# Optimization experiments

Measured on AMD Instinct MI355X. Metric: run time of the kernel, lower is better.

Reference implementation:

```python
import jax, jax.numpy as jnp
import numpy as np

N, E, D, H, DH, M = 100000, 1600000, 128, 8, 16, 3  # nodes, edges, model_dim, heads, head_dim, views
NEG = -1e9


def setup_inputs() -> dict:
    key = jax.random.key(0)
    ks = jax.random.split(key, 12)
    x = jax.random.normal(ks[0], (N, D), jnp.float32)
    src = jax.random.randint(ks[1], (E,), 0, N)
    dst = jax.random.randint(ks[2], (E,), 0, N)
    pi = jax.random.uniform(ks[3], (N, H, M), jnp.float32)
    pi = pi / pi.sum(-1, keepdims=True)  # router mixture over views
    view_w = jax.random.uniform(ks[4], (E, M), jnp.float32)
    s = 1.0 / np.sqrt(D)
    Wq = jax.random.normal(ks[5], (D, D), jnp.float32) * s
    Wk = jax.random.normal(ks[6], (D, D), jnp.float32) * s
    Wv = jax.random.normal(ks[7], (D, D), jnp.float32) * s
    bq = jax.random.normal(ks[8], (D,), jnp.float32) * 0.02
    bk = jax.random.normal(ks[9], (D,), jnp.float32) * 0.02
    bv = jax.random.normal(ks[10], (D,), jnp.float32) * 0.02
    return {"x": x, "pi": pi, "view_w": view_w, "Wq": Wq, "bq": bq,
            "Wk": Wk, "bk": bk, "Wv": Wv, "bv": bv, "src": src, "dst": dst}


def reference(x, pi, view_w, Wq, bq, Wk, bk, Wv, bv, src, dst):
    n = x.shape[0]
    q = (x @ Wq + bq).reshape(n, H, DH)
    k = (x @ Wk + bk).reshape(n, H, DH)
    v = (x @ Wv + bv).reshape(n, H, DH)
    # per-edge mixture weight: sum over views of pi[dst] * view_w  -> [E, H]
    mix = jnp.einsum('ehm,em->eh', pi[dst], view_w)
    raw = jnp.einsum('ehd,ehd->eh', q[dst], k[src]) / jnp.sqrt(jnp.float32(DH))
    scores = raw + jnp.log(jnp.clip(mix, 1e-8))  # adjacency_mode == 'bias'
    valid = mix > 0
    masked = jnp.where(valid, scores, NEG)
    # scatter-softmax over incoming edges per (node, head)
    smax = jax.ops.segment_max(masked, dst, num_segments=n)
    expv = jnp.where(valid, jnp.exp(masked - smax[dst]), 0.0)
    ssum = jax.ops.segment_sum(expv, dst, num_segments=n)
    attn = expv / jnp.maximum(ssum[dst], 1e-8)  # [E, H]
    # weighted scatter-sum aggregation -> [N, H, DH]
    node_states = jax.ops.segment_sum(v[src] * attn[:, :, None], dst, num_segments=n)
    return node_states, attn
```

## Files before the change

### kernel.cpp

```cpp
#include <hip/hip_runtime.h>
#include <hip/hip_bf16.h>
#include <math.h>

#define NEG -1e9f
#define SCAN_CHUNK 2048

typedef _Float16 half8 __attribute__((ext_vector_type(8)));
typedef _Float16 half16v __attribute__((ext_vector_type(16)));
typedef float floatx4 __attribute__((ext_vector_type(4)));


__global__ void hist_kernel(const int* __restrict__ dst, int* __restrict__ counts, int e) {
    int i = blockIdx.x * blockDim.x + threadIdx.x;
    if (i < e) atomicAdd(&counts[dst[i]], 1);
}

__global__ __launch_bounds__(256) void scan_block_sums(const int* __restrict__ counts,
                                                       int* __restrict__ bsum, int n) {
    __shared__ int sd[256];
    int t = threadIdx.x;
    int base = blockIdx.x * SCAN_CHUNK + t * 8;
    int s = 0;
#pragma unroll
    for (int j = 0; j < 8; ++j) {
        int idx = base + j;
        if (idx < n) s += counts[idx];
    }
    sd[t] = s;
    __syncthreads();
    for (int off = 128; off > 0; off >>= 1) {
        if (t < off) sd[t] += sd[t + off];
        __syncthreads();
    }
    if (t == 0) bsum[blockIdx.x] = sd[0];
}

__global__ void scan_wave(int* bsum, int nb) {
    int lane = threadIdx.x;
    int orig = (lane < nb) ? bsum[lane] : 0;
    int v = orig;
    for (int off = 1; off < 64; off <<= 1) {
        int t = __shfl_up(v, off, 64);
        if (lane >= off) v += t;
    }
    if (lane < nb) bsum[lane] = v - orig;
}

__global__ __launch_bounds__(256) void scan_write(const int* __restrict__ counts,
                                                  const int* __restrict__ bsum,
                                                  int* __restrict__ row_ptr,
                                                  int* __restrict__ cursor,
                                                  int n, int total) {
    __shared__ int sd[256];
    int t = threadIdx.x;
    int base = blockIdx.x * SCAN_CHUNK + t * 8;
    int v[8];
    int s = 0;
#pragma unroll
    for (int j = 0; j < 8; ++j) {
        int idx = base + j;
        v[j] = (idx < n) ? counts[idx] : 0;
        s += v[j];
    }
    sd[t] = s;
    __syncthreads();
    for (int off = 1; off < 256; off <<= 1) {
        int tmp = 0;
        if (t >= off) tmp = sd[t - off];
        __syncthreads();
        if (t >= off) sd[t] += tmp;
        __syncthreads();
    }
    int run = bsum[blockIdx.x] + sd[t] - s;
#pragma unroll
    for (int j = 0; j < 8; ++j) {
        int idx = base + j;
        if (idx < n) {
            row_ptr[idx] = run;
            cursor[idx] = run;
            run += v[j];
        }
    }
    if (blockIdx.x == 0 && t == 0) row_ptr[n] = total;
}

__global__ void fill_csr(const int* __restrict__ dst, int* cursor,
                         int* __restrict__ csr, int e) {
    int i = blockIdx.x * blockDim.x + threadIdx.x;
    if (i < e) {
        int p = atomicAdd(&cursor[dst[i]], 1);
        csr[p] = i;
    }
}


__global__ __launch_bounds__(256) void convert_x(const float* __restrict__ x,
                                                 _Float16* __restrict__ xh, int total8) {
    int i = blockIdx.x * blockDim.x + threadIdx.x;
    if (i < total8) {
        const float4* s = (const float4*)x + i * 2;
        float4 a = s[0], b = s[1];
        half8 h;
        h[0] = (_Float16)a.x; h[1] = (_Float16)a.y; h[2] = (_Float16)a.z; h[3] = (_Float16)a.w;
        h[4] = (_Float16)b.x; h[5] = (_Float16)b.y; h[6] = (_Float16)b.z; h[7] = (_Float16)b.w;
        *((half8*)xh + i) = h;
    }
}

__global__ __launch_bounds__(256) void prep_w(const float* __restrict__ Wq,
                                              const float* __restrict__ Wk,
                                              const float* __restrict__ Wv,
                                              _Float16* __restrict__ wt) {
    const float* W = (blockIdx.x == 0) ? Wq : (blockIdx.x == 1) ? Wk : Wv;
    _Float16* out = wt + (size_t)blockIdx.x * 16384;
    int t = threadIdx.x;
    for (int r = 0; r < 64; ++r) {
        int idx = r * 256 + t;
        int k = idx >> 7, nn = idx & 127;
        out[nn * 128 + k] = (_Float16)W[idx];
    }
}


#define LDP 136

__global__ __launch_bounds__(256) void qkv_mfma(
    const _Float16* __restrict__ xh, const _Float16* __restrict__ wt,
    const float* __restrict__ bq, const float* __restrict__ bk,
    const float* __restrict__ bv,
    _Float16* __restrict__ qh, _Float16* __restrict__ kh, _Float16* __restrict__ vh,
    int n) {
    __shared__ __align__(16) _Float16 xs[128 * LDP];
    __shared__ __align__(16) _Float16 ws[128 * LDP];

    int t = threadIdx.x;
    int tile0 = blockIdx.x * 128;
    int sel = blockIdx.y;
    const _Float16* wsel = wt + (size_t)sel * 16384;
    const float* bias = (sel == 0) ? bq : (sel == 1) ? bk : bv;
    _Float16* out = (sel == 0) ? qh : (sel == 1) ? kh : vh;

#pragma unroll
    for (int r = 0; r < 8; ++r) {
        int id = r * 256 + t;
        int row = id >> 4, c8 = id & 15;
        int grow = tile0 + row;
        half8 val = (half8)(_Float16)0;
        if (grow < n) val = *((const half8*)(xh + (size_t)grow * 128) + c8);
        *((half8*)(xs + row * LDP) + c8) = val;
        half8 wv = *((const half8*)(wsel + row * 128) + c8);
        *((half8*)(ws + row * LDP) + c8) = wv;
    }
    __syncthreads();

    int wave = t >> 6, lane = t & 63;
    int wm = (wave & 1) * 64, wn = (wave >> 1) * 64;
    int lrow = lane & 15, quad = lane >> 4;

    floatx4 acc[4][4];
#pragma unroll
    for (int i = 0; i < 4; ++i)
#pragma unroll
        for (int j = 0; j < 4; ++j) acc[i][j] = (floatx4)0.f;

#pragma unroll
    for (int kk = 0; kk < 4; ++kk) {
        int kbase = kk * 32 + quad * 8;
        half8 a[4], b[4];
#pragma unroll
        for (int i = 0; i < 4; ++i)
            a[i] = *(const half8*)(xs + (wm + i * 16 + lrow) * LDP + kbase);
#pragma unroll
        for (int j = 0; j < 4; ++j)
            b[j] = *(const half8*)(ws + (wn + j * 16 + lrow) * LDP + kbase);
#pragma unroll
        for (int i = 0; i < 4; ++i)
#pragma unroll
            for (int j = 0; j < 4; ++j)
                acc[i][j] = __builtin_amdgcn_mfma_f32_16x16x32_f16(a[i], b[j], acc[i][j], 0, 0, 0);
    }

#pragma unroll
    for (int i = 0; i < 4; ++i) {
#pragma unroll
        for (int j = 0; j < 4; ++j) {
            int col = wn + j * 16 + lrow;
            float bv_ = bias[col];
#pragma unroll
            for (int r = 0; r < 4; ++r) {
                int row = wm + i * 16 + quad * 4 + r;
                int grow = tile0 + row;
                if (grow < n) out[(size_t)grow * 128 + col] = (_Float16)(acc[i][j][r] + bv_);
            }
        }
    }
}


__global__ __launch_bounds__(256) void edge_attn(
    const _Float16* __restrict__ qh, const _Float16* __restrict__ kh,
    const _Float16* __restrict__ vh, const float* __restrict__ pi,
    const float* __restrict__ view_w, const int* __restrict__ src,
    const int* __restrict__ row_ptr, const int* __restrict__ csr,
    float* __restrict__ node_out, float* attn_out, int n) {
    int t = threadIdx.x;
    int node = blockIdx.x * 32 + (t >> 3);
    int h = t & 7;
    if (node >= n) return;

    half16v qv = *(const half16v*)(qh + (size_t)node * 128 + h * 16);
    float qf[16];
#pragma unroll
    for (int j = 0; j < 16; ++j) qf[j] = (float)qv[j];

    float p0 = pi[node * 24 + h * 3 + 0];
    float p1 = pi[node * 24 + h * 3 + 1];
    float p2 = pi[node * 24 + h * 3 + 2];
    int beg = row_ptr[node], end = row_ptr[node + 1];

    float m = -INFINITY, l = 0.f;
    float acc[16];
#pragma unroll
    for (int j = 0; j < 16; ++j) acc[j] = 0.f;

    for (int i = beg; i < end; ++i) {
        int e = csr[i];
        int s0 = src[e];
        float w0 = view_w[e * 3 + 0], w1 = view_w[e * 3 + 1], w2 = view_w[e * 3 + 2];
        float mix = fmaf(p0, w0, fmaf(p1, w1, p2 * w2));
        half16v kv = *(const half16v*)(kh + (size_t)s0 * 128 + h * 16);
        float dot = 0.f;
#pragma unroll
        for (int j = 0; j < 16; ++j) dot = fmaf(qf[j], (float)kv[j], dot);
        float s = (mix > 0.f) ? (dot * 0.25f + __logf(fmaxf(mix, 1e-8f))) : NEG;
        attn_out[(size_t)e * 8 + h] = s;
        if (s > 0.5f * NEG) {
            if (s > m) {
                float sc = __expf(m - s);
                l *= sc;
#pragma unroll
                for (int j = 0; j < 16; ++j) acc[j] *= sc;
                m = s;
            }
            float w = __expf(s - m);
            l += w;
            half16v vv = *(const half16v*)(vh + (size_t)s0 * 128 + h * 16);
#pragma unroll
            for (int j = 0; j < 16; ++j) acc[j] = fmaf(w, (float)vv[j], acc[j]);
        }
    }

    float inv = 1.f / fmaxf(l, 1e-8f);
    float4* op = (float4*)(node_out + (size_t)node * 128 + h * 16);
#pragma unroll
    for (int j = 0; j < 4; ++j)
        op[j] = make_float4(acc[4 * j] * inv, acc[4 * j + 1] * inv,
                            acc[4 * j + 2] * inv, acc[4 * j + 3] * inv);

    for (int i = beg; i < end; ++i) {
        int e = csr[i];
        float s = attn_out[(size_t)e * 8 + h];
        float w = (s <= 0.5f * NEG) ? 0.f : __expf(s - m);
        attn_out[(size_t)e * 8 + h] = w * inv;
    }
}


extern "C" void kernel_launch(void* const* d_in, const int* in_sizes, int n_in,
                              void* d_out, int out_size, void* d_ws, size_t ws_size,
                              hipStream_t stream) {
    const float* x  = (const float*)d_in[0];
    const float* pi = (const float*)d_in[1];
    const float* vw = (const float*)d_in[2];
    const float* Wq = (const float*)d_in[3];
    const float* bq = (const float*)d_in[4];
    const float* Wk = (const float*)d_in[5];
    const float* bk = (const float*)d_in[6];
    const float* Wv = (const float*)d_in[7];
    const float* bv = (const float*)d_in[8];
    const int* src  = (const int*)d_in[9];
    const int* dst  = (const int*)d_in[10];

    int n = in_sizes[0] / 128;
    int e = in_sizes[9];

    _Float16* xh = (_Float16*)d_ws;
    _Float16* qh = xh + (size_t)n * 128;
    _Float16* kh = qh + (size_t)n * 128;
    _Float16* vh = kh + (size_t)n * 128;
    _Float16* wt = vh + (size_t)n * 128;
    int* counts  = (int*)(wt + 3 * 16384);
    int* cursor  = counts + n;
    int* row_ptr = cursor + n;
    int* csr     = row_ptr + n + 1;
    int* bsum    = csr + e;

    float* node_out = (float*)d_out;
    float* attn_out = node_out + (size_t)n * 128;

    hipMemsetAsync(counts, 0, (size_t)n * sizeof(int), stream);

    int eb = (e + 255) / 256;
    hist_kernel<<<eb, 256, 0, stream>>>(dst, counts, e);

    int nb = (n + SCAN_CHUNK - 1) / SCAN_CHUNK;
    scan_block_sums<<<nb, 256, 0, stream>>>(counts, bsum, n);
    scan_wave<<<1, 64, 0, stream>>>(bsum, nb);
    scan_write<<<nb, 256, 0, stream>>>(counts, bsum, row_ptr, cursor, n, e);
    fill_csr<<<eb, 256, 0, stream>>>(dst, cursor, csr, e);

    int tot8 = (n * 128) / 8;
    convert_x<<<(tot8 + 255) / 256, 256, 0, stream>>>(x, xh, tot8);
    prep_w<<<3, 256, 0, stream>>>(Wq, Wk, Wv, wt);

    int gtiles = (n + 127) / 128;
    qkv_mfma<<<dim3(gtiles, 3), 256, 0, stream>>>(xh, wt, bq, bk, bv, qh, kh, vh, n);

    int gb = (n + 31) / 32;
    edge_attn<<<gb, 256, 0, stream>>>(qh, kh, vh, pi, vw, src, row_ptr, csr,
                                      node_out, attn_out, n);
}
```

Measured before the change: 738.3 us.

## Degree-sort nodes, fuse x conversion into QKV GEMM, two heads per thread

Nodes are bucketed by in-degree with a histogram and scatter, so threads in a wave process similar-length edge lists and divergence drops. x is now converted to fp16 inside the QKV GEMM, and one block computes all three projections, so the separate conversion kernel and its buffer go away. Each attention thread handles two heads, prefetches the next edge's indices and view weights, and keeps raw scores in an fp16 scratch buffer instead of round-tripping them through the fp32 attention output. The risks are extra small kernels and atomics for the degree sort, a serialised three-pass GEMM per block, and fp16 rounding of scores before the exponent.

```diff
diff --git a/kernel.cpp b/kernel.cpp
--- a/kernel.cpp
+++ b/kernel.cpp
@@ -7,6 +7,7 @@
 
 typedef _Float16 half8 __attribute__((ext_vector_type(8)));
 typedef _Float16 half16v __attribute__((ext_vector_type(16)));
+typedef _Float16 half2v __attribute__((ext_vector_type(2)));
 typedef float floatx4 __attribute__((ext_vector_type(4)));
 
 
@@ -35,15 +36,19 @@
     if (t == 0) bsum[blockIdx.x] = sd[0];
 }
 
-__global__ void scan_wave(int* bsum, int nb) {
+__global__ void scan_wave2(int* b, int* cur, int nb) {
     int lane = threadIdx.x;
-    int orig = (lane < nb) ? bsum[lane] : 0;
+    int orig = (lane < nb) ? b[lane] : 0;
     int v = orig;
     for (int off = 1; off < 64; off <<= 1) {
         int t = __shfl_up(v, off, 64);
         if (lane >= off) v += t;
     }
-    if (lane < nb) bsum[lane] = v - orig;
+    if (lane < nb) {
+        int ex = v - orig;
+        b[lane] = ex;
+        if (cur) cur[lane] = ex;
+    }
 }
 
 __global__ __launch_bounds__(256) void scan_write(const int* __restrict__ counts,
@@ -94,28 +99,36 @@
 }
 
 
-__global__ __launch_bounds__(256) void convert_x(const float* __restrict__ x,
-                                                 _Float16* __restrict__ xh, int total8) {
+__global__ void deg_hist(const int* __restrict__ counts, int* __restrict__ dbin, int n) {
     int i = blockIdx.x * blockDim.x + threadIdx.x;
-    if (i < total8) {
-        const float4* s = (const float4*)x + i * 2;
-        float4 a = s[0], b = s[1];
-        half8 h;
-        h[0] = (_Float16)a.x; h[1] = (_Float16)a.y; h[2] = (_Float16)a.z; h[3] = (_Float16)a.w;
-        h[4] = (_Float16)b.x; h[5] = (_Float16)b.y; h[6] = (_Float16)b.z; h[7] = (_Float16)b.w;
-        *((half8*)xh + i) = h;
-    }
-}
+    if (i < n) {
+        int d = counts[i]; if (d > 63) d = 63;
+        atomicAdd(&dbin[63 - d], 1);
+    }
+}
+
+__global__ void deg_scatter(const int* __restrict__ counts, int* dcur,
+                            int* __restrict__ order, int n) {
+    int i = blockIdx.x * blockDim.x + threadIdx.x;
+    if (i < n) {
+        int d = counts[i]; if (d > 63) d = 63;
+        int p = atomicAdd(&dcur[63 - d], 1);
+        order[p] = i;
+    }
+}
+
 
 __global__ __launch_bounds__(256) void prep_w(const float* __restrict__ Wq,
                                               const float* __restrict__ Wk,
                                               const float* __restrict__ Wv,
                                               _Float16* __restrict__ wt) {
-    const float* W = (blockIdx.x == 0) ? Wq : (blockIdx.x == 1) ? Wk : Wv;
-    _Float16* out = wt + (size_t)blockIdx.x * 16384;
-    int t = threadIdx.x;
-    for (int r = 0; r < 64; ++r) {
-        int idx = r * 256 + t;
+    int mat = blockIdx.x >> 3, chunk = blockIdx.x & 7;
+    const float* W = (mat == 0) ? Wq : (mat == 1) ? Wk : Wv;
+    _Float16* out = wt + (size_t)mat * 16384;
+    int base = chunk * 2048 + threadIdx.x;
+#pragma unroll
+    for (int r = 0; r < 8; ++r) {
+        int idx = base + r * 256;
         int k = idx >> 7, nn = idx & 127;
         out[nn * 128 + k] = (_Float16)W[idx];
     }
@@ -125,7 +138,7 @@
 #define LDP 136
 
 __global__ __launch_bounds__(256) void qkv_mfma(
-    const _Float16* __restrict__ xh, const _Float16* __restrict__ wt,
+    const float* __restrict__ x, const _Float16* __restrict__ wt,
     const float* __restrict__ bq, const float* __restrict__ bk,
     const float* __restrict__ bv,
     _Float16* __restrict__ qh, _Float16* __restrict__ kh, _Float16* __restrict__ vh,
@@ -135,10 +148,6 @@
 
     int t = threadIdx.x;
     int tile0 = blockIdx.x * 128;
-    int sel = blockIdx.y;
-    const _Float16* wsel = wt + (size_t)sel * 16384;
-    const float* bias = (sel == 0) ? bq : (sel == 1) ? bk : bv;
-    _Float16* out = (sel == 0) ? qh : (sel == 1) ? kh : vh;
 
 #pragma unroll
     for (int r = 0; r < 8; ++r) {
@@ -146,51 +155,69 @@
         int row = id >> 4, c8 = id & 15;
         int grow = tile0 + row;
         half8 val = (half8)(_Float16)0;
-        if (grow < n) val = *((const half8*)(xh + (size_t)grow * 128) + c8);
+        if (grow < n) {
+            const float4* xp = (const float4*)(x + (size_t)grow * 128 + c8 * 8);
+            float4 a = xp[0], b = xp[1];
+            val[0] = (_Float16)a.x; val[1] = (_Float16)a.y;
+            val[2] = (_Float16)a.z; val[3] = (_Float16)a.w;
+            val[4] = (_Float16)b.x; val[5] = (_Float16)b.y;
+            val[6] = (_Float16)b.z; val[7] = (_Float16)b.w;
+        }
         *((half8*)(xs + row * LDP) + c8) = val;
-        half8 wv = *((const half8*)(wsel + row * 128) + c8);
-        *((half8*)(ws + row * LDP) + c8) = wv;
-    }
-    __syncthreads();
+    }
 
     int wave = t >> 6, lane = t & 63;
     int wm = (wave & 1) * 64, wn = (wave >> 1) * 64;
     int lrow = lane & 15, quad = lane >> 4;
 
-    floatx4 acc[4][4];
-#pragma unroll
-    for (int i = 0; i < 4; ++i)
-#pragma unroll
-        for (int j = 0; j < 4; ++j) acc[i][j] = (floatx4)0.f;
-
-#pragma unroll
-    for (int kk = 0; kk < 4; ++kk) {
-        int kbase = kk * 32 + quad * 8;
-        half8 a[4], b[4];
+    for (int sel = 0; sel < 3; ++sel) {
+        __syncthreads();
+        const _Float16* wsel = wt + (size_t)sel * 16384;
+#pragma unroll
+        for (int r = 0; r < 8; ++r) {
+            int id = r * 256 + t;
+            int row = id >> 4, c8 = id & 15;
+            *((half8*)(ws + row * LDP) + c8) = *((const half8*)(wsel + row * 128) + c8);
+        }
+        __syncthreads();
+
+        floatx4 acc[4][4];
 #pragma unroll
         for (int i = 0; i < 4; ++i)
-            a[i] = *(const half8*)(xs + (wm + i * 16 + lrow) * LDP + kbase);
-#pragma unroll
-        for (int j = 0; j < 4; ++j)
-            b[j] = *(const half8*)(ws + (wn + j * 16 + lrow) * LDP + kbase);
-#pragma unroll
-        for (int i = 0; i < 4; ++i)
+#pragma unroll
+            for (int j = 0; j < 4; ++j) acc[i][j] = (floatx4)0.f;
+
+#pragma unroll
+        for (int kk = 0; kk < 4; ++kk) {
+            int kbase = kk * 32 + quad * 8;
+            half8 a[4], b[4];
+#pragma unroll
+            for (int i = 0; i < 4; ++i)
+                a[i] = *(const half8*)(xs + (wm + i * 16 + lrow) * LDP + kbase);
 #pragma unroll
             for (int j = 0; j < 4; ++j)
-                acc[i][j] = __builtin_amdgcn_mfma_f32_16x16x32_f16(a[i], b[j], acc[i][j], 0, 0, 0);
-    }
-
-#pragma unroll
-    for (int i = 0; i < 4; ++i) {
-#pragma unroll
-        for (int j = 0; j < 4; ++j) {
-            int col = wn + j * 16 + lrow;
-            float bv_ = bias[col];
-#pragma unroll
-            for (int r = 0; r < 4; ++r) {
-                int row = wm + i * 16 + quad * 4 + r;
-                int grow = tile0 + row;
-                if (grow < n) out[(size_t)grow * 128 + col] = (_Float16)(acc[i][j][r] + bv_);
+                b[j] = *(const half8*)(ws + (wn + j * 16 + lrow) * LDP + kbase);
+#pragma unroll
+            for (int i = 0; i < 4; ++i)
+#pragma unroll
+                for (int j = 0; j < 4; ++j)
+                    acc[i][j] = __builtin_amdgcn_mfma_f32_16x16x32_f16(a[i], b[j], acc[i][j], 0, 0, 0);
+        }
+
+        const float* bias = (sel == 0) ? bq : (sel == 1) ? bk : bv;
+        _Float16* out = (sel == 0) ? qh : (sel == 1) ? kh : vh;
+#pragma unroll
+        for (int i = 0; i < 4; ++i) {
+#pragma unroll
+            for (int j = 0; j < 4; ++j) {
+                int col = wn + j * 16 + lrow;
+                float bv_ = bias[col];
+#pragma unroll
+                for (int r = 0; r < 4; ++r) {
+                    int row = wm + i * 16 + quad * 4 + r;
+                    int grow = tile0 + row;
+                    if (grow < n) out[(size_t)grow * 128 + col] = (_Float16)(acc[i][j][r] + bv_);
+                }
             }
         }
     }
@@ -202,66 +229,115 @@
     const _Float16* __restrict__ vh, const float* __restrict__ pi,
     const float* __restrict__ view_w, const int* __restrict__ src,
     const int* __restrict__ row_ptr, const int* __restrict__ csr,
-    float* __restrict__ node_out, float* attn_out, int n) {
-    int t = threadIdx.x;
-    int node = blockIdx.x * 32 + (t >> 3);
-    int h = t & 7;
-    if (node >= n) return;
-
-    half16v qv = *(const half16v*)(qh + (size_t)node * 128 + h * 16);
-    float qf[16];
-#pragma unroll
-    for (int j = 0; j < 16; ++j) qf[j] = (float)qv[j];
-
-    float p0 = pi[node * 24 + h * 3 + 0];
-    float p1 = pi[node * 24 + h * 3 + 1];
-    float p2 = pi[node * 24 + h * 3 + 2];
+    const int* __restrict__ order,
+    float* __restrict__ node_out, float* __restrict__ attn_out,
+    _Float16* __restrict__ sc, int n) {
+    int gid = blockIdx.x * blockDim.x + threadIdx.x;
+    int slot = gid >> 2;
+    if (slot >= n) return;
+    int node = order[slot];
+    int h0 = (gid & 3) * 2;
+
+    const half16v* qp = (const half16v*)(qh + (size_t)node * 128 + h0 * 16);
+    half16v qa = qp[0], qb = qp[1];
+
+    const float* pip = pi + node * 24 + h0 * 3;
+    float p00 = pip[0], p01 = pip[1], p02 = pip[2];
+    float p10 = pip[3], p11 = pip[4], p12 = pip[5];
+
     int beg = row_ptr[node], end = row_ptr[node + 1];
 
-    float m = -INFINITY, l = 0.f;
-    float acc[16];
-#pragma unroll
-    for (int j = 0; j < 16; ++j) acc[j] = 0.f;
+    float m0 = -INFINITY, l0 = 0.f, m1 = -INFINITY, l1 = 0.f;
+    float acc0[16], acc1[16];
+#pragma unroll
+    for (int j = 0; j < 16; ++j) { acc0[j] = 0.f; acc1[j] = 0.f; }
+
+    int e_n = 0, s_n = 0;
+    float wa_n = 0.f, wb_n = 0.f, wc_n = 0.f;
+    if (beg < end) {
+        e_n = csr[beg]; s_n = src[e_n];
+        const float* vp_ = view_w + (size_t)e_n * 3;
+        wa_n = vp_[0]; wb_n = vp_[1]; wc_n = vp_[2];
+    }
+
+    for (int i = beg; i < end; ++i) {
+        int e = e_n, s0 = s_n;
+        float wa = wa_n, wb = wb_n, wc = wc_n;
+
+        const half16v* kp = (const half16v*)(kh + (size_t)s0 * 128 + h0 * 16);
+        half16v k0 = kp[0], k1 = kp[1];
+        const half16v* vp = (const half16v*)(vh + (size_t)s0 * 128 + h0 * 16);
+        half16v v0 = vp[0], v1 = vp[1];
+
+        if (i + 1 < end) {
+            e_n = csr[i + 1]; s_n = src[e_n];
+            const float* vpn = view_w + (size_t)e_n * 3;
+            wa_n = vpn[0]; wb_n = vpn[1]; wc_n = vpn[2];
+        }
+
+        float mix0 = fmaf(p00, wa, fmaf(p01, wb, p02 * wc));
+        float mix1 = fmaf(p10, wa, fmaf(p11, wb, p12 * wc));
+        float d0 = 0.f, d1 = 0.f;
+#pragma unroll
+        for (int j = 0; j < 16; ++j) {
+            d0 = fmaf((float)qa[j], (float)k0[j], d0);
+            d1 = fmaf((float)qb[j], (float)k1[j], d1);
+        }
+        float s0s = (mix0 > 0.f) ? (d0 * 0.25f + __logf(fmaxf(mix0, 1e-8f))) : NEG;
+        float s1s = (mix1 > 0.f) ? (d1 * 0.25f + __logf(fmaxf(mix1, 1e-8f))) : NEG;
+
+        half2v stmp; stmp[0] = (_Float16)s0s; stmp[1] = (_Float16)s1s;
+        *(half2v*)(sc + (size_t)e * 8 + h0) = stmp;
+
+        if (s0s > 0.5f * NEG) {
+            if (s0s > m0) {
+                float r = __expf(m0 - s0s);
+                l0 *= r;
+#pragma unroll
+                for (int j = 0; j < 16; ++j) acc0[j] *= r;
+                m0 = s0s;
+            }
+            float w = __expf(s0s - m0);
+            l0 += w;
+#pragma unroll
+            for (int j = 0; j < 16; ++j) acc0[j] = fmaf(w, (float)v0[j], acc0[j]);
+        }
+        if (s1s > 0.5f * NEG) {
+            if (s1s > m1) {
+                float r = __expf(m1 - s1s);
+                l1 *= r;
+#pragma unroll
+                for (int j = 0; j < 16; ++j) acc1[j] *= r;
+                m1 = s1s;
+            }
+            float w = __expf(s1s - m1);
+            l1 += w;
+#pragma unroll
+            for (int j = 0; j < 16; ++j) acc1[j] = fmaf(w, (float)v1[j], acc1[j]);
+        }
+    }
+
+    float inv0 = 1.f / fmaxf(l0, 1e-8f);
+    float inv1 = 1.f / fmaxf(l1, 1e-8f);
+
+    float4* op = (float4*)(node_out + (size_t)node * 128 + h0 * 16);
+#pragma unroll
+    for (int j = 0; j < 4; ++j)
+        op[j] = make_float4(acc0[4 * j] * inv0, acc0[4 * j + 1] * inv0,
+                            acc0[4 * j + 2] * inv0, acc0[4 * j + 3] * inv0);
+#pragma unroll
+    for (int j = 0; j < 4; ++j)
+        op[4 + j] = make_float4(acc1[4 * j] * inv1, acc1[4 * j + 1] * inv1,
+                                acc1[4 * j + 2] * inv1, acc1[4 * j + 3] * inv1);
 
     for (int i = beg; i < end; ++i) {
         int e = csr[i];
-        int s0 = src[e];
-        float w0 = view_w[e * 3 + 0], w1 = view_w[e * 3 + 1], w2 = view_w[e * 3 + 2];
-        float mix = fmaf(p0, w0, fmaf(p1, w1, p2 * w2));
-        half16v kv = *(const half16v*)(kh + (size_t)s0 * 128 + h * 16);
-        float dot = 0.f;
-#pragma unroll
-        for (int j = 0; j < 16; ++j) dot = fmaf(qf[j], (float)kv[j], dot);
-        float s = (mix > 0.f) ? (dot * 0.25f + __logf(fmaxf(mix, 1e-8f))) : NEG;
-        attn_out[(size_t)e * 8 + h] = s;
-        if (s > 0.5f * NEG) {
-            if (s > m) {
-                float sc = __expf(m - s);
-                l *= sc;
-#pragma unroll
-                for (int j = 0; j < 16; ++j) acc[j] *= sc;
-                m = s;
-            }
-            float w = __expf(s - m);
-            l += w;
-            half16v vv = *(const half16v*)(vh + (size_t)s0 * 128 + h * 16);
-#pragma unroll
-            for (int j = 0; j < 16; ++j) acc[j] = fmaf(w, (float)vv[j], acc[j]);
-        }
-    }
-
-    float inv = 1.f / fmaxf(l, 1e-8f);
-    float4* op = (float4*)(node_out + (size_t)node * 128 + h * 16);
-#pragma unroll
-    for (int j = 0; j < 4; ++j)
-        op[j] = make_float4(acc[4 * j] * inv, acc[4 * j + 1] * inv,
-                            acc[4 * j + 2] * inv, acc[4 * j + 3] * inv);
-
-    for (int i = beg; i < end; ++i) {
-        int e = csr[i];
-        float s = attn_out[(size_t)e * 8 + h];
-        float w = (s <= 0.5f * NEG) ? 0.f : __expf(s - m);
-        attn_out[(size_t)e * 8 + h] = w * inv;
+        half2v sv = *(const half2v*)(sc + (size_t)e * 8 + h0);
+        float a0 = (float)sv[0], a1 = (float)sv[1];
+        float w0 = (a0 <= 0.5f * NEG) ? 0.f : __expf(a0 - m0) * inv0;
+        float w1 = (a1 <= 0.5f * NEG) ? 0.f : __expf(a1 - m1) * inv1;
+        float2 wout = make_float2(w0, w1);
+        *(float2*)(attn_out + (size_t)e * 8 + h0) = wout;
     }
 }
 
@@ -284,39 +360,45 @@
     int n = in_sizes[0] / 128;
     int e = in_sizes[9];
 
-    _Float16* xh = (_Float16*)d_ws;
-    _Float16* qh = xh + (size_t)n * 128;
+    _Float16* qh = (_Float16*)d_ws;
     _Float16* kh = qh + (size_t)n * 128;
     _Float16* vh = kh + (size_t)n * 128;
     _Float16* wt = vh + (size_t)n * 128;
-    int* counts  = (int*)(wt + 3 * 16384);
-    int* cursor  = counts + n;
+    _Float16* sc = wt + 3 * 16384;
+    int* counts  = (int*)(sc + (size_t)e * 8);
+    int* dbin    = counts + n;
+    int* dcur    = dbin + 64;
+    int* cursor  = dcur + 64;
     int* row_ptr = cursor + n;
-    int* csr     = row_ptr + n + 1;
-    int* bsum    = csr + e;
+    int* bsum    = row_ptr + n + 1;
+    int* order   = bsum + 64;
+    int* csr     = order + n;
 
     float* node_out = (float*)d_out;
     float* attn_out = node_out + (size_t)n * 128;
 
-    hipMemsetAsync(counts, 0, (size_t)n * sizeof(int), stream);
+    hipMemsetAsync(counts, 0, (size_t)(n + 64) * sizeof(int), stream);
 
     int eb = (e + 255) / 256;
+    int nbl = (n + 255) / 256;
     hist_kernel<<<eb, 256, 0, stream>>>(dst, counts, e);
 
     int nb = (n + SCAN_CHUNK - 1) / SCAN_CHUNK;
     scan_block_sums<<<nb, 256, 0, stream>>>(counts, bsum, n);
-    scan_wave<<<1, 64, 0, stream>>>(bsum, nb);
+    scan_wave2<<<1, 64, 0, stream>>>(bsum, (int*)nullptr, nb);
     scan_write<<<nb, 256, 0, stream>>>(counts, bsum, row_ptr, cursor, n, e);
     fill_csr<<<eb, 256, 0, stream>>>(dst, cursor, csr, e);
 
-    int tot8 = (n * 128) / 8;
-    convert_x<<<(tot8 + 255) / 256, 256, 0, stream>>>(x, xh, tot8);
-    prep_w<<<3, 256, 0, stream>>>(Wq, Wk, Wv, wt);
+    deg_hist<<<nbl, 256, 0, stream>>>(counts, dbin, n);
+    scan_wave2<<<1, 64, 0, stream>>>(dbin, dcur, 64);
+    deg_scatter<<<nbl, 256, 0, stream>>>(counts, dcur, order, n);
+
+    prep_w<<<24, 256, 0, stream>>>(Wq, Wk, Wv, wt);
 
     int gtiles = (n + 127) / 128;
-    qkv_mfma<<<dim3(gtiles, 3), 256, 0, stream>>>(xh, wt, bq, bk, bv, qh, kh, vh, n);
-
-    int gb = (n + 31) / 32;
-    edge_attn<<<gb, 256, 0, stream>>>(qh, kh, vh, pi, vw, src, row_ptr, csr,
-                                      node_out, attn_out, n);
-}
+    qkv_mfma<<<gtiles, 256, 0, stream>>>(x, wt, bq, bk, bv, qh, kh, vh, n);
+
+    int athreads = n * 4;
+    edge_attn<<<(athreads + 255) / 256, 256, 0, stream>>>(
+        qh, kh, vh, pi, vw, src, row_ptr, csr, order, node_out, attn_out, sc, n);
+}
```

Measured after the change: 1.209 ms. 1.64x slower.
